# Performance work log

Hardware: AMD Instinct MI355X
Metric: run time of the kernel (lower is better)

## Reference

```python
import jax, jax.numpy as jnp
import numpy as np

N, E, DIN, HID, G, L = 50000, 200000, 128, 128, 64, 6
H1, H2 = 8, 4
EPS_LN, EPS_BN = 1e-5, 1e-5


def setup_inputs() -> dict:
    key = jax.random.key(0)
    ks = iter(jax.random.split(key, 32))
    def nrm(shape, scale=0.05):
        return jax.random.normal(next(ks), shape, dtype=jnp.float32) * scale
    z = lambda *s: jnp.zeros(s, jnp.float32)
    o = lambda *s: jnp.ones(s, jnp.float32)
    return {
        'x': jax.random.normal(next(ks), (N, DIN), dtype=jnp.float32),
        'edge_index': jax.random.randint(next(ks), (2, E), 0, N),
        'batch': jnp.sort(jax.random.randint(next(ks), (N,), 0, G)),
        'W1': nrm((DIN, H1 * HID)), 'a_src1': nrm((H1, HID)), 'a_dst1': nrm((H1, HID)), 'b1': z(H1 * HID),
        'W2': nrm((H1 * HID, H2 * HID)), 'a_src2': nrm((H2, HID)), 'a_dst2': nrm((H2, HID)), 'b2': z(H2 * HID),
        'W3': nrm((H2 * HID, HID)), 'b3': z(HID),
        'wq': nrm((L, HID, HID)), 'bq': z(L, HID), 'wk': nrm((L, HID, HID)), 'bk': z(L, HID),
        'wv': nrm((L, HID, HID)), 'bv': z(L, HID), 'wo': nrm((L, HID, HID)), 'bo': z(L, HID),
        'ln1g': o(L, HID), 'ln1b': z(L, HID), 'ln2g': o(L, HID), 'ln2b': z(L, HID),
        'wf1': nrm((L, HID, 4 * HID)), 'bf1': z(L, 4 * HID), 'wf2': nrm((L, 4 * HID, HID)), 'bf2': z(L, HID),
        'bn1_g': o(2 * HID), 'bn1_b': z(2 * HID),
        'fc1_w': nrm((2 * HID, HID // 2)), 'fc1_b': z(HID // 2),
        'bn2_g': o(HID // 2), 'bn2_b': z(HID // 2),
        'fc2_w': nrm((HID // 2, 2)), 'fc2_b': z(2),
    }


def _ln(x, g, b):
    mu = x.mean(-1, keepdims=True)
    v = ((x - mu) ** 2).mean(-1, keepdims=True)
    return (x - mu) * jax.lax.rsqrt(v + EPS_LN) * g + b


def _gat(x, src, dst, W, a_s, a_d, b, heads):
    # PyG GATConv: message src -> dst, segment softmax over incoming edges per dst.
    h = (x @ W).reshape(x.shape[0], heads, -1)           # [N, H, C]
    e = jax.nn.leaky_relu((h * a_s).sum(-1)[src] + (h * a_d).sum(-1)[dst], 0.2)  # [E, H]
    m = jax.ops.segment_max(e, dst, num_segments=N)
    ex = jnp.exp(e - jnp.where(jnp.isfinite(m), m, 0.0)[dst])
    s = jax.ops.segment_sum(ex, dst, num_segments=N)
    alpha = ex / (s[dst] + 1e-16)
    out = jax.ops.segment_sum(alpha[:, :, None] * h[src], dst, num_segments=N)
    return out.reshape(N, -1) + b


def _forward(x, edge_index, batch, W1, a_src1, a_dst1, b1, W2, a_src2, a_dst2, b2, W3, b3,
             wq, bq, wk, bk, wv, bv, wo, bo, ln1g, ln1b, ln2g, ln2b, wf1, bf1, wf2, bf2,
             bn1_g, bn1_b, fc1_w, fc1_b, bn2_g, bn2_b, fc2_w, fc2_b):
    loop = jnp.arange(N, dtype=edge_index.dtype)
    src = jnp.concatenate([edge_index[0], loop])          # add self-loops (PyG default)
    dst = jnp.concatenate([edge_index[1], loop])
    h = jax.nn.elu(_gat(x, src, dst, W1, a_src1, a_dst1, b1, H1))
    h = jax.nn.elu(_gat(h, src, dst, W2, a_src2, a_dst2, b2, H2))
    # GCNConv with symmetric normalization (self-loops already included)
    deg = jax.ops.segment_sum(jnp.ones(src.shape, h.dtype), dst, num_segments=N)
    dinv = jnp.where(deg > 0, jax.lax.rsqrt(jnp.maximum(deg, 1e-12)), 0.0)
    norm = dinv[src] * dinv[dst]
    h = jax.nn.elu(jax.ops.segment_sum(norm[:, None] * (h @ W3)[src], dst, num_segments=N) + b3)
    # TransformerEncoder over seq_len=1 (h3.unsqueeze(1)): softmax over one key == 1,
    # so MHA output == Wo @ (Wv h + bv) + bo exactly; q/k have no effect on the output.
    for l in range(L):
        sa = (h @ wv[l] + bv[l]) @ wo[l] + bo[l]
        h = _ln(h + sa, ln1g[l], ln1b[l])
        ff = jax.nn.gelu(h @ wf1[l] + bf1[l], approximate=False) @ wf2[l] + bf2[l]
        h = _ln(h + ff, ln2g[l], ln2b[l])
    # global mean / max pool over graphs
    cnt = jax.ops.segment_sum(jnp.ones((N,), h.dtype), batch, num_segments=G)
    hm = jax.ops.segment_sum(h, batch, num_segments=G) / jnp.maximum(cnt, 1.0)[:, None]
    hx = jax.ops.segment_max(h, batch, num_segments=G)
    hx = jnp.where(jnp.isfinite(hx), hx, 0.0)
    hc = jnp.concatenate([hm, hx], axis=1)                # [G, 2*HID]
    bn_s = 1.0 / np.sqrt(1.0 + EPS_BN)                    # eval BN: running stats (0, 1)
    hc = hc * bn_s * bn1_g + bn1_b
    hc = jax.nn.elu(hc @ fc1_w + fc1_b)
    hc = hc * bn_s * bn2_g + bn2_b
    return hc @ fc2_w + fc2_b                             # [G, 2]


def reference(x, edge_index, batch, W1, a_src1, a_dst1, b1, W2, a_src2, a_dst2, b2, W3, b3,
              wq, bq, wk, bk, wv, bv, wo, bo, ln1g, ln1b, ln2g, ln2b, wf1, bf1, wf2, bf2,
              bn1_g, bn1_b, fc1_w, fc1_b, bn2_g, bn2_b, fc2_w, fc2_b):
    return _forward(x, edge_index, batch, W1, a_src1, a_dst1, b1, W2, a_src2, a_dst2, b2, W3, b3,
                    wq, bq, wk, bk, wv, bv, wo, bo, ln1g, ln1b, ln2g, ln2b, wf1, bf1, wf2, bf2,
                    bn1_g, bn1_b, fc1_w, fc1_b, bn2_g, bn2_b, fc2_w, fc2_b)
```

## Files before the change

### kernel.cpp

```cpp
#include <hip/hip_runtime.h>
#include <hip/hip_bf16.h>
#include <math.h>

#define NN 50000
#define EE 200000
#define ET 250000
#define GG 64
#define LL 6

using short8 = __attribute__((ext_vector_type(8))) short;
using f32x4  = __attribute__((ext_vector_type(4))) float;
typedef unsigned short ushortT;

__device__ __forceinline__ float elu1(float x) { return x > 0.f ? x : expm1f(x); }
__device__ __forceinline__ float gelu_exact(float x) {
    return 0.5f * x * (1.f + erff(x * 0.70710678118654752440f));
}
__device__ __forceinline__ short f2bf(float f) {
    __hip_bfloat16 h = __float2bfloat16(f);
    return *reinterpret_cast<short*>(&h);
}
__device__ __forceinline__ float bf2f(ushortT u) {
    return __uint_as_float(((unsigned)u) << 16);
}
__device__ __forceinline__ void accum8(float* acc, float a, uint4 d) {
    acc[0] += a * bf2f((ushortT)(d.x & 0xffff));
    acc[1] += a * bf2f((ushortT)(d.x >> 16));
    acc[2] += a * bf2f((ushortT)(d.y & 0xffff));
    acc[3] += a * bf2f((ushortT)(d.y >> 16));
    acc[4] += a * bf2f((ushortT)(d.z & 0xffff));
    acc[5] += a * bf2f((ushortT)(d.z >> 16));
    acc[6] += a * bf2f((ushortT)(d.w & 0xffff));
    acc[7] += a * bf2f((ushortT)(d.w >> 16));
}

__global__ void count_deg_kernel(const int* __restrict__ ei, int* __restrict__ deg) {
    int e = blockIdx.x * 256 + threadIdx.x;
    if (e >= ET) return;
    int dst = (e < EE) ? ei[EE + e] : (e - EE);
    atomicAdd(&deg[dst], 1);
}

__global__ void scan_kernel(const int* __restrict__ deg, int* __restrict__ row_ptr, int n) {
    __shared__ int s[1024];
    int tid = threadIdx.x;
    const int per = (n + 1023) / 1024;
    int lo = tid * per, hi = min(lo + per, n);
    int sum = 0;
    for (int i = lo; i < hi; i++) sum += deg[i];
    s[tid] = sum;
    __syncthreads();
    for (int off = 1; off < 1024; off <<= 1) {
        int t = (tid >= off) ? s[tid - off] : 0;
        __syncthreads();
        s[tid] += t;
        __syncthreads();
    }
    int run = s[tid] - sum;
    for (int i = lo; i < hi; i++) { row_ptr[i] = run; run += deg[i]; }
    if (tid == 1023) row_ptr[n] = s[1023];
}

__global__ void fill_csr_kernel(const int* __restrict__ ei, const int* __restrict__ row_ptr,
                                int* __restrict__ cursor, int* __restrict__ edge_src) {
    int e = blockIdx.x * 256 + threadIdx.x;
    if (e >= ET) return;
    int src, dst;
    if (e < EE) { src = ei[e]; dst = ei[EE + e]; }
    else        { src = e - EE; dst = e - EE; }
    int pos = atomicAdd(&cursor[dst], 1);
    edge_src[row_ptr[dst] + pos] = src;
}

__global__ void dinv_kernel(const int* __restrict__ row_ptr, float* __restrict__ dinv) {
    int n = blockIdx.x * 256 + threadIdx.x;
    if (n >= NN) return;
    int d = row_ptr[n + 1] - row_ptr[n];
    dinv[n] = (d > 0) ? rsqrtf((float)d) : 0.f;
}

__global__ __launch_bounds__(256) void local_sort_kernel(
    const int* __restrict__ row_ptr, int* __restrict__ perm, int n_nodes) {
    int g = blockIdx.x * 4 + (threadIdx.x >> 6);
    int l = threadIdx.x & 63;
    int node = g * 64 + l;
    if (g * 64 >= n_nodes) return;
    int d = (node < n_nodes) ? (row_ptr[node + 1] - row_ptr[node]) : 0x7fffffff;
    int rank = 0;
#pragma unroll 16
    for (int j = 0; j < 64; j++) {
        int dj = __shfl(d, j);
        rank += (dj < d) || (dj == d && j < l);
    }
    if (node < n_nodes) perm[g * 64 + rank] = node;
}

__global__ void wvwo_kernel(const float* __restrict__ wv, const float* __restrict__ wo,
                            const float* __restrict__ bv, const float* __restrict__ bo,
                            float* __restrict__ Wvo, float* __restrict__ bvo) {
    int l = blockIdx.y;
    const float* Wv = wv + l * 16384;
    const float* Wo = wo + l * 16384;
    int tid = blockIdx.x * 256 + threadIdx.x;
    if (tid < 16384) {
        int r = tid >> 7, c = tid & 127;
        float s = 0.f;
        for (int k = 0; k < 128; k++) s += Wv[r * 128 + k] * Wo[k * 128 + c];
        Wvo[l * 16384 + tid] = s;
    }
    if (blockIdx.x == 0 && threadIdx.x < 128) {
        int c = threadIdx.x;
        float s = bo[l * 128 + c];
        for (int k = 0; k < 128; k++) s += bv[l * 128 + k] * Wo[k * 128 + c];
        bvo[l * 128 + c] = s;
    }
}

__global__ void bprep_kernel(const float* __restrict__ B, short* __restrict__ Bp,
                             int K, int N, int ldb, long srcStride) {
    int layer = blockIdx.y;
    const float* Bsrc = B + srcStride * layer;
    short* Bd = Bp + (size_t)K * N * layer;
    int total = (K >> 5) * (N >> 4) * 64;
    int tid = blockIdx.x * 256 + threadIdx.x;
    if (tid >= total) return;
    int l = tid & 63;
    int rest = tid >> 6;
    int kbc = K >> 5;
    int kb = rest % kbc;
    int c16 = rest / kbc;
    int n = c16 * 16 + (l & 15);
    int kbase = kb * 32 + (l >> 4) * 8;
    short v[8];
#pragma unroll
    for (int j = 0; j < 8; j++) v[j] = f2bf(Bsrc[(size_t)(kbase + j) * ldb + n]);
    *(uint4*)(Bd + (size_t)tid * 8) = *(uint4*)v;
}

__global__ void cast_bf16_kernel(const float* __restrict__ in, short* __restrict__ out, int n4) {
    int i = blockIdx.x * 256 + threadIdx.x;
    if (i >= n4) return;
    float4 v = *(const float4*)(in + (size_t)i * 4);
    short s[4] = { f2bf(v.x), f2bf(v.y), f2bf(v.z), f2bf(v.w) };
    *(uint2*)(out + (size_t)i * 4) = *(uint2*)s;
}

template <int EPI, bool BIAS, bool OUTBF16, int NSPLIT, int KBC,
          bool TMAJ = false, bool ATILE32 = false>
__global__ __launch_bounds__(256) void gemm_bf16_kernel(
    const short* __restrict__ A, const short* __restrict__ Bp,
    const float* __restrict__ bias, void* __restrict__ Cv,
    const float* __restrict__ a_s, const float* __restrict__ a_d,
    float* __restrict__ as_out, float* __restrict__ ad_out, int asH,
    int M, int K, int Nc) {
    __shared__ short Bs[(KBC > 0) ? KBC * 4096 : 8192];
    int t = threadIdx.x;
    int w = t >> 6, l = t & 63;
    int ln = l & 15, lq = l >> 4;
    int MBceil = (M + 63) >> 6;
    int bx = blockIdx.x;
    int xcd = bx & 7, idx = bx >> 3;
    int t2 = idx % NSPLIT;
    int mb = (idx / NSPLIT) * 8 + xcd;
    if (mb >= MBceil) return;
    int bm = mb * 64 + w * 16;
    int arow = bm + ln;
    bool aok = arow < M;
    int rowb = bm + lq * 4;
    const short* Ap = A + (size_t)arow * K + lq * 8;

    auto aload = [&](int kb) -> short8 {
        if (!aok) return (short8){0, 0, 0, 0, 0, 0, 0, 0};
        const short* p;
        if constexpr (ATILE32)
            p = A + ((size_t)kb * M + arow) * 32 + lq * 8;
        else
            p = Ap + kb * 32;
        return *(const short8*)p;
    };

    f32x4 acc[8];
#pragma unroll
    for (int j = 0; j < 8; j++) acc[j] = (f32x4){0.f, 0.f, 0.f, 0.f};

    if constexpr (KBC > 0) {
        {
            const uint4* src = (const uint4*)(Bp + (size_t)t2 * KBC * 4096);
            uint4* dst = (uint4*)Bs;
#pragma unroll
            for (int i = 0; i < KBC * 2; i++)
                dst[i * 256 + t] = src[i * 256 + t];
        }
        short8 af[KBC];
#pragma unroll
        for (int kb = 0; kb < KBC; kb++)
            af[kb] = aload(kb);
        __syncthreads();
#pragma unroll
        for (int kb = 0; kb < KBC; kb++)
#pragma unroll
            for (int ct = 0; ct < 8; ct++) {
                short8 bfr = *(const short8*)(Bs + ((ct * KBC + kb) * 64 + l) * 8);
                acc[ct] = __builtin_amdgcn_mfma_f32_16x16x32_bf16(af[kb], bfr, acc[ct], 0, 0, 0);
            }
    } else {
        int kbc = K >> 5;
        int sct = t >> 5, spart = t & 31;
        auto stage = [&](int buf, int kb) {
            const uint4* src = (const uint4*)(Bp + ((size_t)(t2 * 8 + sct) * kbc + kb) * 512);
            uint4* dst = (uint4*)(Bs + buf * 4096 + sct * 512);
            dst[spart * 2]     = src[spart * 2];
            dst[spart * 2 + 1] = src[spart * 2 + 1];
        };
        stage(0, 0);
        __syncthreads();
        for (int kb = 0; kb < kbc; kb++) {
            if (kb + 1 < kbc) stage((kb + 1) & 1, kb + 1);
            short8 af = aload(kb);
            const short* bsb = Bs + (kb & 1) * 4096;
#pragma unroll
            for (int ct = 0; ct < 8; ct++) {
                short8 bfr = *(const short8*)(bsb + (ct * 64 + l) * 8);
                acc[ct] = __builtin_amdgcn_mfma_f32_16x16x32_bf16(af, bfr, acc[ct], 0, 0, 0);
            }
            __syncthreads();
        }
    }

    if (EPI == 2) {
        const float* asv = a_s + t2 * 128;
        const float* adv = a_d + t2 * 128;
#pragma unroll
        for (int reg = 0; reg < 4; reg++) {
            float vs = 0.f, vd = 0.f;
#pragma unroll
            for (int ct = 0; ct < 8; ct++) {
                int colL = ct * 16 + ln;
                float av = acc[ct][reg];
                vs += av * asv[colL];
                vd += av * adv[colL];
            }
            vs += __shfl_xor(vs, 1); vs += __shfl_xor(vs, 2);
            vs += __shfl_xor(vs, 4); vs += __shfl_xor(vs, 8);
            vd += __shfl_xor(vd, 1); vd += __shfl_xor(vd, 2);
            vd += __shfl_xor(vd, 4); vd += __shfl_xor(vd, 8);
            int row = rowb + reg;
            if (ln == 0 && row < M) {
                as_out[(size_t)row * asH + t2] = vs;
                ad_out[(size_t)row * asH + t2] = vd;
            }
        }
    }
#pragma unroll
    for (int ct = 0; ct < 8; ct++) {
        int col = t2 * 128 + ct * 16 + ln;
        float bv_ = BIAS ? bias[col] : 0.f;
#pragma unroll
        for (int reg = 0; reg < 4; reg++) {
            int row = rowb + reg;
            if (row < M) {
                float v = acc[ct][reg] + bv_;
                if (OUTBF16) {
                    size_t addr;
                    if constexpr (TMAJ)
                        addr = ((size_t)(col >> 5) * M + row) * 32 + (col & 31);
                    else
                        addr = (size_t)row * Nc + col;
                    ((__hip_bfloat16*)Cv)[addr] = __float2bfloat16(v);
                } else {
                    ((float*)Cv)[(size_t)row * Nc + col] = v;
                }
            }
        }
    }
}

#define TS 136
__global__ __launch_bounds__(256) void transformer_fused_kernel(
    const short* __restrict__ Qb, const short* __restrict__ Wvop,
    const float* __restrict__ bvo, const short* __restrict__ wf1p,
    const short* __restrict__ wf2p, const float* __restrict__ bf1,
    const float* __restrict__ bf2, const float* __restrict__ ln1g,
    const float* __restrict__ ln1b, const float* __restrict__ ln2g,
    const float* __restrict__ ln2b, float* __restrict__ fQ, int M) {
    __shared__ short Ts[4][16 * TS];
    int t = threadIdx.x;
    int w = t >> 6, l = t & 63;
    int ln = l & 15, lq = l >> 4;
    int MBceil = (M + 63) >> 6;
    int bx = blockIdx.x;
    int xcd = bx & 7, mb = (bx >> 3) * 8 + xcd;
    if (mb >= MBceil) return;
    int bm = mb * 64 + w * 16;
    int rowb = bm + lq * 4;
    short* Tw = &Ts[w][0];

    ushortT hc[8][4];
#pragma unroll
    for (int ct = 0; ct < 8; ct++) {
        int col = ct * 16 + ln;
#pragma unroll
        for (int reg = 0; reg < 4; reg++) {
            int row = rowb + reg;
            hc[ct][reg] = (row < M) ? ((const ushortT*)Qb)[(size_t)row * 128 + col] : 0;
        }
    }

    auto bounceA = [&](short8* a) {
#pragma unroll
        for (int ct = 0; ct < 8; ct++)
#pragma unroll
            for (int reg = 0; reg < 4; reg++)
                Tw[(lq * 4 + reg) * TS + ct * 16 + ln] = (short)hc[ct][reg];
#pragma unroll
        for (int kb = 0; kb < 4; kb++)
            a[kb] = *(const short8*)(Tw + ln * TS + kb * 32 + lq * 8);
    };
    auto bload = [&](const short* wp, int frag) -> short8 {
        return *(const short8*)(wp + ((size_t)frag * 64 + l) * 8);
    };
    auto lnEpi = [&](f32x4* acc, const float* bias, const float* g,
                     const float* b, bool writeF) {
        float v[8][4];
#pragma unroll
        for (int ct = 0; ct < 8; ct++) {
            float bv_ = bias[ct * 16 + ln];
#pragma unroll
            for (int reg = 0; reg < 4; reg++)
                v[ct][reg] = acc[ct][reg] + bv_ + bf2f(hc[ct][reg]);
        }
#pragma unroll
        for (int reg = 0; reg < 4; reg++) {
            float s = 0.f;
#pragma unroll
            for (int ct = 0; ct < 8; ct++) s += v[ct][reg];
            s += __shfl_xor(s, 1); s += __shfl_xor(s, 2);
            s += __shfl_xor(s, 4); s += __shfl_xor(s, 8);
            float mean = s * (1.f / 128.f);
            float s2 = 0.f;
#pragma unroll
            for (int ct = 0; ct < 8; ct++) { float d = v[ct][reg] - mean; s2 += d * d; }
            s2 += __shfl_xor(s2, 1); s2 += __shfl_xor(s2, 2);
            s2 += __shfl_xor(s2, 4); s2 += __shfl_xor(s2, 8);
            float rstd = rsqrtf(s2 * (1.f / 128.f) + 1e-5f);
            int row = rowb + reg;
#pragma unroll
            for (int ct = 0; ct < 8; ct++) {
                int col = ct * 16 + ln;
                float o = (v[ct][reg] - mean) * rstd * g[col] + b[col];
                hc[ct][reg] = (ushortT)f2bf(o);
                if (writeF && row < M) fQ[(size_t)row * 128 + col] = o;
            }
        }
    };

    for (int lay = 0; lay < LL; lay++) {
        short8 a1[4];
        bounceA(a1);
        const short* wvl = Wvop + (size_t)lay * 16384;
        f32x4 acc1[8];
#pragma unroll
        for (int j = 0; j < 8; j++) acc1[j] = (f32x4){0.f, 0.f, 0.f, 0.f};
#pragma unroll
        for (int kb = 0; kb < 4; kb++)
#pragma unroll
            for (int ct = 0; ct < 8; ct++) {
                short8 bfr = bload(wvl, ct * 4 + kb);
                acc1[ct] = __builtin_amdgcn_mfma_f32_16x16x32_bf16(a1[kb], bfr, acc1[ct], 0, 0, 0);
            }
        lnEpi(acc1, bvo + lay * 128, ln1g + lay * 128, ln1b + lay * 128, false);

        short8 af1[4];
        bounceA(af1);
        const short* w1l = wf1p + (size_t)lay * 65536;
        const short* w2l = wf2p + (size_t)lay * 65536;
        f32x4 acc2[8];
#pragma unroll
        for (int j = 0; j < 8; j++) acc2[j] = (f32x4){0.f, 0.f, 0.f, 0.f};
        for (int kc = 0; kc < 4; kc++) {
            f32x4 acct[8];
#pragma unroll
            for (int j = 0; j < 8; j++) acct[j] = (f32x4){0.f, 0.f, 0.f, 0.f};
#pragma unroll
            for (int kb = 0; kb < 4; kb++)
#pragma unroll
                for (int ct = 0; ct < 8; ct++) {
                    short8 bfr = bload(w1l, kc * 32 + ct * 4 + kb);
                    acct[ct] = __builtin_amdgcn_mfma_f32_16x16x32_bf16(af1[kb], bfr, acct[ct], 0, 0, 0);
                }
            const float* bfc = bf1 + lay * 512 + kc * 128;
#pragma unroll
            for (int ct = 0; ct < 8; ct++) {
                float bv = bfc[ct * 16 + ln];
#pragma unroll
                for (int reg = 0; reg < 4; reg++)
                    Tw[(lq * 4 + reg) * TS + ct * 16 + ln] = f2bf(gelu_exact(acct[ct][reg] + bv));
            }
            short8 a2[4];
#pragma unroll
            for (int kb2 = 0; kb2 < 4; kb2++)
                a2[kb2] = *(const short8*)(Tw + ln * TS + kb2 * 32 + lq * 8);
#pragma unroll
            for (int kb2 = 0; kb2 < 4; kb2++)
#pragma unroll
                for (int ct = 0; ct < 8; ct++) {
                    short8 bfr = bload(w2l, ct * 16 + kc * 4 + kb2);
                    acc2[ct] = __builtin_amdgcn_mfma_f32_16x16x32_bf16(a2[kb2], bfr, acc2[ct], 0, 0, 0);
                }
        }
        lnEpi(acc2, bf2 + lay * 128, ln2g + lay * 128, ln2b + lay * 128, lay == LL - 1);
    }
}

template <int H>
__global__ __launch_bounds__(256) void gat_alpha_kernel(
    const float* __restrict__ as_, const float* __restrict__ ad_,
    const int* __restrict__ row_ptr, const int* __restrict__ edge_src,
    float* __restrict__ exA, float* __restrict__ exS, int n_nodes) {
    const int GS = 64 / H;
    int node = blockIdx.x * 4 + (threadIdx.x >> 6);
    if (node >= n_nodes) return;
    int l = threadIdx.x & 63;
    int h = l / GS;
    int lig = l % GS;
    int start = row_ptr[node];
    int deg = row_ptr[node + 1] - start;
    float adn = ad_[(size_t)node * H + h];
    float m = -1e30f;
    for (int j = lig; j < deg; j += GS) {
        int s = edge_src[start + j];
        float e = as_[(size_t)s * H + h] + adn;
        e = e > 0.f ? e : 0.2f * e;
        m = fmaxf(m, e);
    }
#pragma unroll
    for (int mask = 1; mask < GS; mask <<= 1)
        m = fmaxf(m, __shfl_xor(m, mask));
    float S = 0.f;
    for (int j = lig; j < deg; j += GS) {
        int s = edge_src[start + j];
        float e = as_[(size_t)s * H + h] + adn;
        e = e > 0.f ? e : 0.2f * e;
        float ex = expf(e - m);
        exA[(size_t)h * ET + (start + j)] = ex;
        S += ex;
    }
#pragma unroll
    for (int mask = 1; mask < GS; mask <<= 1)
        S += __shfl_xor(S, mask);
    if (lig == 0) exS[(size_t)h * n_nodes + node] = S;
}

__global__ __launch_bounds__(256) void gat_agg_tiled_kernel(
    const ushortT* __restrict__ hT, const float* __restrict__ exA,
    const float* __restrict__ exS, const float* __restrict__ bias,
    const int* __restrict__ row_ptr, const int* __restrict__ edge_src,
    const int* __restrict__ perm,
    __hip_bfloat16* __restrict__ outT, int n_nodes, int NB) {
    int bx = blockIdx.x;
    int xcd = bx & 7, rest = bx >> 3;
    int tl = rest / NB, nb = rest - tl * NB;
    int tile = tl * 8 + xcd;
    int nl = threadIdx.x >> 2, q = threadIdx.x & 3;
    int idx = nb * 64 + nl;
    if (idx >= n_nodes) return;
    int node = perm[idx];
    int hb = tile >> 2;
    const ushortT* __restrict__ base = hT + (size_t)tile * n_nodes * 32 + q * 8;
    const float* __restrict__ exAh = exA + (size_t)hb * ET;
    int start = row_ptr[node];
    int deg = row_ptr[node + 1] - start;
    float acc[8];
#pragma unroll
    for (int c = 0; c < 8; c++) acc[c] = 0.f;
    for (int j = 0; j < deg; j++) {
        int s = edge_src[start + j];
        float a = exAh[start + j];
        uint4 d = *(const uint4*)(base + (size_t)s * 32);
        accum8(acc, a, d);
    }
    float inv = 1.f / (exS[(size_t)hb * n_nodes + node] + 1e-16f);
    const float* bp = bias + tile * 32 + q * 8;
    short o[8];
#pragma unroll
    for (int c = 0; c < 8; c++)
        o[c] = f2bf(elu1(acc[c] * inv + bp[c]));
    *(uint4*)(outT + ((size_t)tile * n_nodes + node) * 32 + q * 8) = *(uint4*)o;
}

__global__ __launch_bounds__(256, 2) void gcn_agg_kernel(
    const ushortT* __restrict__ hp, const float* __restrict__ dinv,
    const float* __restrict__ b3, const int* __restrict__ row_ptr,
    const int* __restrict__ edge_src,
    __hip_bfloat16* __restrict__ outb, int n_nodes) {
    int node = blockIdx.x * 2 + (threadIdx.x >> 7);
    int c = threadIdx.x & 127;
    if (node >= n_nodes) return;
    int start = row_ptr[node];
    int deg = row_ptr[node + 1] - start;
    float dn = dinv[node];
    float acc = 0.f;
    auto LS = [&](int j) { return edge_src[start + min(j, deg - 1)]; };
    int s0 = LS(0), s1 = LS(1), s2 = LS(2), s3 = LS(3);
    int s4 = LS(4), s5 = LS(5), s6 = LS(6), s7 = LS(7);
    auto HW = [&](int s, int j, float& h, float& w) {
        h = bf2f(hp[(size_t)s * 128 + c]);
        w = (j < deg) ? dinv[s] * dn : 0.f;
    };
    float h0, h1, h2, h3, h4, h5, h6, h7;
    float w0, w1, w2, w3, w4, w5, w6, w7;
    HW(s0, 0, h0, w0); HW(s1, 1, h1, w1); HW(s2, 2, h2, w2); HW(s3, 3, h3, w3);
    HW(s4, 4, h4, w4); HW(s5, 5, h5, w5); HW(s6, 6, h6, w6); HW(s7, 7, h7, w7);
    int j0 = 0;
    while (true) {
        int jn = j0 + 8;
        bool more = jn < deg;
        float g0, g1, g2, g3, g4, g5, g6, g7;
        float v0 = 0.f, v1 = 0.f, v2 = 0.f, v3 = 0.f;
        float v4 = 0.f, v5 = 0.f, v6 = 0.f, v7 = 0.f;
        if (more) {
            int t0 = LS(jn),     t1 = LS(jn + 1), t2 = LS(jn + 2), t3 = LS(jn + 3);
            int t4 = LS(jn + 4), t5 = LS(jn + 5), t6 = LS(jn + 6), t7 = LS(jn + 7);
            HW(t0, jn,     g0, v0); HW(t1, jn + 1, g1, v1);
            HW(t2, jn + 2, g2, v2); HW(t3, jn + 3, g3, v3);
            HW(t4, jn + 4, g4, v4); HW(t5, jn + 5, g5, v5);
            HW(t6, jn + 6, g6, v6); HW(t7, jn + 7, g7, v7);
        }
        acc += w0 * h0 + w1 * h1 + w2 * h2 + w3 * h3
             + w4 * h4 + w5 * h5 + w6 * h6 + w7 * h7;
        if (!more) break;
        h0 = g0; h1 = g1; h2 = g2; h3 = g3;
        h4 = g4; h5 = g5; h6 = g6; h7 = g7;
        w0 = v0; w1 = v1; w2 = v2; w3 = v3;
        w4 = v4; w5 = v5; w6 = v6; w7 = v7;
        j0 = jn;
    }
    outb[(size_t)node * 128 + c] = __float2bfloat16(elu1(acc + b3[c]));
}

__global__ void pool1_kernel(const float* __restrict__ Q, const int* __restrict__ batch,
                             float* __restrict__ psum, float* __restrict__ pmax, int n_nodes) {
    int g = blockIdx.x, seg = blockIdx.y;
    int c = threadIdx.x;
    int lo, hi;
    {
        int l = 0, h = n_nodes;
        while (l < h) { int mid = (l + h) >> 1; if (batch[mid] < g) l = mid + 1; else h = mid; }
        lo = l;
        l = lo; h = n_nodes;
        while (l < h) { int mid = (l + h) >> 1; if (batch[mid] < g + 1) l = mid + 1; else h = mid; }
        hi = l;
    }
    int len = hi - lo;
    int a = lo + (int)((long)len * seg / 8);
    int b = lo + (int)((long)len * (seg + 1) / 8);
    float s = 0.f, mx = -INFINITY;
    for (int n = a; n < b; n++) {
        float v = Q[(size_t)n * 128 + c];
        s += v;
        mx = fmaxf(mx, v);
    }
    psum[(g * 8 + seg) * 128 + c] = s;
    pmax[(g * 8 + seg) * 128 + c] = mx;
}

__global__ void pool2_kernel(const float* __restrict__ psum, const float* __restrict__ pmax,
                             const int* __restrict__ batch,
                             const float* __restrict__ bn1g, const float* __restrict__ bn1b,
                             float* __restrict__ hc, int n_nodes) {
    int g = blockIdx.x;
    int c = threadIdx.x;
    int lo, hi;
    {
        int l = 0, h = n_nodes;
        while (l < h) { int mid = (l + h) >> 1; if (batch[mid] < g) l = mid + 1; else h = mid; }
        lo = l;
        l = lo; h = n_nodes;
        while (l < h) { int mid = (l + h) >> 1; if (batch[mid] < g + 1) l = mid + 1; else h = mid; }
        hi = l;
    }
    int cnt = hi - lo;
    float s = 0.f, mx = -INFINITY;
    for (int seg = 0; seg < 8; seg++) {
        s += psum[(g * 8 + seg) * 128 + c];
        mx = fmaxf(mx, pmax[(g * 8 + seg) * 128 + c]);
    }
    float hm = s / fmaxf((float)cnt, 1.f);
    float hx = (cnt > 0 && isfinite(mx)) ? mx : 0.f;
    const float bn_s = 0.99999500003749968f;
    hc[g * 256 + c]       = hm * bn_s * bn1g[c] + bn1b[c];
    hc[g * 256 + 128 + c] = hx * bn_s * bn1g[128 + c] + bn1b[128 + c];
}

__global__ void head_kernel(const float* __restrict__ hc,
                            const float* __restrict__ fc1w, const float* __restrict__ fc1b,
                            const float* __restrict__ bn2g, const float* __restrict__ bn2b,
                            const float* __restrict__ fc2w, const float* __restrict__ fc2b,
                            float* __restrict__ out) {
    int g = blockIdx.x;
    int j = threadIdx.x;
    const float bn_s = 0.99999500003749968f;
    float acc = fc1b[j];
    for (int i = 0; i < 256; i++) acc += hc[g * 256 + i] * fc1w[i * 64 + j];
    acc = elu1(acc);
    acc = acc * bn_s * bn2g[j] + bn2b[j];
    __shared__ float sv[64];
    sv[j] = acc;
    __syncthreads();
    if (j < 2) {
        float o = fc2b[j];
        for (int i = 0; i < 64; i++) o += sv[i] * fc2w[i * 2 + j];
        out[g * 2 + j] = o;
    }
}

extern "C" void kernel_launch(void* const* d_in, const int* in_sizes, int n_in,
                              void* d_out, int out_size, void* d_ws, size_t ws_size,
                              hipStream_t stream) {
    const float* x    = (const float*)d_in[0];
    const int*   ei   = (const int*)d_in[1];
    const int*   batch= (const int*)d_in[2];
    const float* W1   = (const float*)d_in[3];
    const float* as1  = (const float*)d_in[4];
    const float* ad1  = (const float*)d_in[5];
    const float* b1   = (const float*)d_in[6];
    const float* W2   = (const float*)d_in[7];
    const float* as2  = (const float*)d_in[8];
    const float* ad2  = (const float*)d_in[9];
    const float* b2   = (const float*)d_in[10];
    const float* W3   = (const float*)d_in[11];
    const float* b3   = (const float*)d_in[12];
    const float* wv   = (const float*)d_in[17];
    const float* bv   = (const float*)d_in[18];
    const float* wo   = (const float*)d_in[19];
    const float* bo   = (const float*)d_in[20];
    const float* ln1g = (const float*)d_in[21];
    const float* ln1b = (const float*)d_in[22];
    const float* ln2g = (const float*)d_in[23];
    const float* ln2b = (const float*)d_in[24];
    const float* wf1  = (const float*)d_in[25];
    const float* bf1  = (const float*)d_in[26];
    const float* wf2  = (const float*)d_in[27];
    const float* bf2  = (const float*)d_in[28];
    const float* bn1g = (const float*)d_in[29];
    const float* bn1b = (const float*)d_in[30];
    const float* fc1w = (const float*)d_in[31];
    const float* fc1b = (const float*)d_in[32];
    const float* bn2g = (const float*)d_in[33];
    const float* bn2b = (const float*)d_in[34];
    const float* fc2w = (const float*)d_in[35];
    const float* fc2b = (const float*)d_in[36];
    float* out = (float*)d_out;

    char* wsb = (char*)d_ws;
    short* xb    = (short*)wsb;
    float* exAf  = (float*)wsb;
    float* exSf  = (float*)(wsb + 8000000);
    short* h1t   = (short*)(wsb + 12800000);
    short* h2t   = (short*)(wsb + 12800000);
    short* h3pre = (short*)(wsb + 12800000);
    short* bh1   = (short*)(wsb + 115200000);
    short* bh2   = (short*)(wsb + 115200000);
    float* fQ    = (float*)(wsb + 128000000);
    short* Qb    = (short*)(wsb + 153600000);
    char* tail = wsb + 217600000;
    short* W1p  = (short*)tail;  tail += 262144;
    short* W2p  = (short*)tail;  tail += 1048576;
    short* W3p  = (short*)tail;  tail += 131072;
    short* Wvop = (short*)tail;  tail += 196608;
    short* wf1p = (short*)tail;  tail += 786432;
    short* wf2p = (short*)tail;  tail += 786432;
    float* Wvo  = (float*)tail;  tail += 393216;
    float* bvo  = (float*)tail;  tail += 3072;
    float* fAS  = (float*)tail;  tail += 1600000;
    float* fAD  = (float*)tail;  tail += 1600000;
    float* fDv  = (float*)tail;  tail += 200000;
    float* psum = (float*)tail;  tail += 262144;
    float* pmax = (float*)tail;  tail += 262144;
    float* fHC  = (float*)tail;  tail += 65536;
    int* iDeg   = (int*)tail;    tail += 200000;
    int* iRP    = (int*)tail;    tail += 200004;
    int* iCur   = (int*)tail;    tail += 200000;
    int* iES    = (int*)tail;    tail += 1000000;

    hipMemsetAsync(iDeg, 0, NN * sizeof(int), stream);
    hipMemsetAsync(iCur, 0, NN * sizeof(int), stream);

    count_deg_kernel<<<(ET + 255) / 256, 256, 0, stream>>>(ei, iDeg);
    scan_kernel<<<1, 1024, 0, stream>>>(iDeg, iRP, NN);
    fill_csr_kernel<<<(ET + 255) / 256, 256, 0, stream>>>(ei, iRP, iCur, iES);
    dinv_kernel<<<(NN + 255) / 256, 256, 0, stream>>>(iRP, fDv);
    int* perm = iCur;
    local_sort_kernel<<<(NN / 64 + 4) / 4, 256, 0, stream>>>(iRP, perm, NN);

    wvwo_kernel<<<dim3(64, 6), 256, 0, stream>>>(wv, wo, bv, bo, Wvo, bvo);
    auto bprep = [&](const float* B, short* Bp, int K, int N, int ldb, long sStride, int layers) {
        int total = (K >> 5) * (N >> 4) * 64;
        dim3 grid((total + 255) / 256, layers);
        bprep_kernel<<<grid, 256, 0, stream>>>(B, Bp, K, N, ldb, sStride);
    };
    bprep(W1, W1p, 128, 1024, 1024, 0, 1);
    bprep(W2, W2p, 1024, 512, 512, 0, 1);
    bprep(W3, W3p, 512, 128, 128, 0, 1);
    bprep(Wvo, Wvop, 128, 128, 128, 16384, 6);
    bprep(wf1, wf1p, 128, 512, 512, 65536, 6);
    bprep(wf2, wf2p, 512, 128, 128, 65536, 6);
    cast_bf16_kernel<<<(NN * 128 / 4 + 255) / 256, 256, 0, stream>>>(x, xb, NN * 128 / 4);

    const int MB64 = (NN + 63) / 64;
    const int MBp = ((MB64 + 7) / 8) * 8;
    const int NB = (NN + 63) / 64;

    gemm_bf16_kernel<2, false, true, 8, 4, true, false><<<MBp * 8, 256, 0, stream>>>(
        xb, W1p, nullptr, h1t, as1, ad1, fAS, fAD, 8, NN, 128, 1024);
    gat_alpha_kernel<8><<<(NN + 3) / 4, 256, 0, stream>>>(
        fAS, fAD, iRP, iES, exAf, exSf, NN);
    gat_agg_tiled_kernel<<<4 * NB * 8, 256, 0, stream>>>(
        (const ushortT*)h1t, exAf, exSf, b1, iRP, iES, perm, (__hip_bfloat16*)bh1, NN, NB);
    gemm_bf16_kernel<2, false, true, 4, 0, true, true><<<MBp * 4, 256, 0, stream>>>(
        bh1, W2p, nullptr, h2t, as2, ad2, fAS, fAD, 4, NN, 1024, 512);
    gat_alpha_kernel<4><<<(NN + 3) / 4, 256, 0, stream>>>(
        fAS, fAD, iRP, iES, exAf, exSf, NN);
    gat_agg_tiled_kernel<<<2 * NB * 8, 256, 0, stream>>>(
        (const ushortT*)h2t, exAf, exSf, b2, iRP, iES, perm, (__hip_bfloat16*)bh2, NN, NB);
    gemm_bf16_kernel<0, false, true, 1, 0, false, true><<<MBp, 256, 0, stream>>>(
        bh2, W3p, nullptr, h3pre, nullptr, nullptr, nullptr, nullptr, 0, NN, 512, 128);
    gcn_agg_kernel<<<(NN + 1) / 2, 256, 0, stream>>>(
        (const ushortT*)h3pre, fDv, b3, iRP, iES, (__hip_bfloat16*)Qb, NN);
    transformer_fused_kernel<<<MBp, 256, 0, stream>>>(
        Qb, Wvop, bvo, wf1p, wf2p, bf1, bf2, ln1g, ln1b, ln2g, ln2b, fQ, NN);
    pool1_kernel<<<dim3(GG, 8), 128, 0, stream>>>(fQ, batch, psum, pmax, NN);
    pool2_kernel<<<GG, 128, 0, stream>>>(psum, pmax, batch, bn1g, bn1b, fHC, NN);
    head_kernel<<<GG, 64, 0, stream>>>(fHC, fc1w, fc1b, bn2g, bn2b, fc2w, fc2b, out);
}
```

Before: 1.373 ms.

## Stage transformer weights through double-buffered LDS with async global-to-LDS prefetch

```diff
diff --git a/kernel.cpp b/kernel.cpp
--- a/kernel.cpp
+++ b/kernel.cpp
@@ -32,6 +32,16 @@
     acc[5] += a * bf2f((ushortT)(d.z >> 16));
     acc[6] += a * bf2f((ushortT)(d.w & 0xffff));
     acc[7] += a * bf2f((ushortT)(d.w >> 16));
+}
+
+__device__ __forceinline__ void gl16(const short* g, short* l) {
+#if defined(__has_builtin) && __has_builtin(__builtin_amdgcn_global_load_lds)
+    __builtin_amdgcn_global_load_lds(
+        (const __attribute__((address_space(1))) unsigned int*)g,
+        (__attribute__((address_space(3))) unsigned int*)l, 16, 0, 0);
+#else
+    *(uint4*)l = *(const uint4*)g;
+#endif
 }
 
 __global__ void count_deg_kernel(const int* __restrict__ ei, int* __restrict__ deg) {
@@ -283,6 +293,7 @@
     const float* __restrict__ bf2, const float* __restrict__ ln1g,
     const float* __restrict__ ln1b, const float* __restrict__ ln2g,
     const float* __restrict__ ln2b, float* __restrict__ fQ, int M) {
+    __shared__ short BsD[16384];
     __shared__ short Ts[4][16 * TS];
     int t = threadIdx.x;
     int w = t >> 6, l = t & 63;
@@ -306,6 +317,32 @@
         }
     }
 
+    auto pfLinear = [&](const short* base, int buf) {
+#pragma unroll
+        for (int i = 0; i < 4; i++) {
+            int off = i * 2048 + w * 512;
+            gl16(base + off + l * 8, BsD + buf * 8192 + off);
+        }
+    };
+    auto pfW2 = [&](const short* w2l, int kc, int h, int buf) {
+#pragma unroll
+        for (int i = 0; i < 4; i++) {
+            int frag = ((i + h * 4) << 4) + kc * 4 + w;
+            int slot = i * 4 + w;
+            gl16(w2l + frag * 512 + l * 8, BsD + buf * 8192 + slot * 512);
+        }
+    };
+    auto mfmaHalf = [&](f32x4* acc, int half, short8* a, int buf) {
+        const short* bsb = BsD + buf * 8192;
+#pragma unroll
+        for (int kb = 0; kb < 4; kb++)
+#pragma unroll
+            for (int ct2 = 0; ct2 < 4; ct2++) {
+                short8 bfr = *(const short8*)(bsb + ((ct2 * 4 + kb) * 64 + l) * 8);
+                acc[half * 4 + ct2] =
+                    __builtin_amdgcn_mfma_f32_16x16x32_bf16(a[kb], bfr, acc[half * 4 + ct2], 0, 0, 0);
+            }
+    };
     auto bounceA = [&](short8* a) {
 #pragma unroll
         for (int ct = 0; ct < 8; ct++)
@@ -315,9 +352,6 @@
 #pragma unroll
         for (int kb = 0; kb < 4; kb++)
             a[kb] = *(const short8*)(Tw + ln * TS + kb * 32 + lq * 8);
-    };
-    auto bload = [&](const short* wp, int frag) -> short8 {
-        return *(const short8*)(wp + ((size_t)frag * 64 + l) * 8);
     };
     auto lnEpi = [&](f32x4* acc, const float* bias, const float* g,
                      const float* b, bool writeF) {
@@ -354,26 +388,29 @@
         }
     };
 
+    int cur = 0;
+    pfLinear(Wvop, 0);
+    __syncthreads();
+
     for (int lay = 0; lay < LL; lay++) {
+        const short* wvl = Wvop + (size_t)lay * 16384;
+        const short* w1l = wf1p + (size_t)lay * 65536;
+        const short* w2l = wf2p + (size_t)lay * 65536;
         short8 a1[4];
         bounceA(a1);
-        const short* wvl = Wvop + (size_t)lay * 16384;
         f32x4 acc1[8];
 #pragma unroll
         for (int j = 0; j < 8; j++) acc1[j] = (f32x4){0.f, 0.f, 0.f, 0.f};
-#pragma unroll
-        for (int kb = 0; kb < 4; kb++)
-#pragma unroll
-            for (int ct = 0; ct < 8; ct++) {
-                short8 bfr = bload(wvl, ct * 4 + kb);
-                acc1[ct] = __builtin_amdgcn_mfma_f32_16x16x32_bf16(a1[kb], bfr, acc1[ct], 0, 0, 0);
-            }
+        pfLinear(wvl + 8192, cur ^ 1);
+        mfmaHalf(acc1, 0, a1, cur);
+        __syncthreads(); cur ^= 1;
+        pfLinear(w1l, cur ^ 1);
+        mfmaHalf(acc1, 1, a1, cur);
         lnEpi(acc1, bvo + lay * 128, ln1g + lay * 128, ln1b + lay * 128, false);
-
         short8 af1[4];
         bounceA(af1);
-        const short* w1l = wf1p + (size_t)lay * 65536;
-        const short* w2l = wf2p + (size_t)lay * 65536;
+        __syncthreads(); cur ^= 1;
+
         f32x4 acc2[8];
 #pragma unroll
         for (int j = 0; j < 8; j++) acc2[j] = (f32x4){0.f, 0.f, 0.f, 0.f};
@@ -381,13 +418,11 @@
             f32x4 acct[8];
 #pragma unroll
             for (int j = 0; j < 8; j++) acct[j] = (f32x4){0.f, 0.f, 0.f, 0.f};
-#pragma unroll
-            for (int kb = 0; kb < 4; kb++)
-#pragma unroll
-                for (int ct = 0; ct < 8; ct++) {
-                    short8 bfr = bload(w1l, kc * 32 + ct * 4 + kb);
-                    acct[ct] = __builtin_amdgcn_mfma_f32_16x16x32_bf16(af1[kb], bfr, acct[ct], 0, 0, 0);
-                }
+            pfLinear(w1l + kc * 16384 + 8192, cur ^ 1);
+            mfmaHalf(acct, 0, af1, cur);
+            __syncthreads(); cur ^= 1;
+            pfW2(w2l, kc, 0, cur ^ 1);
+            mfmaHalf(acct, 1, af1, cur);
             const float* bfc = bf1 + lay * 512 + kc * 128;
 #pragma unroll
             for (int ct = 0; ct < 8; ct++) {
@@ -400,13 +435,14 @@
 #pragma unroll
             for (int kb2 = 0; kb2 < 4; kb2++)
                 a2[kb2] = *(const short8*)(Tw + ln * TS + kb2 * 32 + lq * 8);
-#pragma unroll
-            for (int kb2 = 0; kb2 < 4; kb2++)
-#pragma unroll
-                for (int ct = 0; ct < 8; ct++) {
-                    short8 bfr = bload(w2l, ct * 16 + kc * 4 + kb2);
-                    acc2[ct] = __builtin_amdgcn_mfma_f32_16x16x32_bf16(a2[kb2], bfr, acc2[ct], 0, 0, 0);
-                }
+            __syncthreads(); cur ^= 1;
+            pfW2(w2l, kc, 1, cur ^ 1);
+            mfmaHalf(acc2, 0, a2, cur);
+            __syncthreads(); cur ^= 1;
+            if (kc < 3)            pfLinear(w1l + (kc + 1) * 16384, cur ^ 1);
+            else if (lay < LL - 1) pfLinear(Wvop + (size_t)(lay + 1) * 16384, cur ^ 1);
+            mfmaHalf(acc2, 1, a2, cur);
+            __syncthreads(); cur ^= 1;
         }
         lnEpi(acc2, bf2 + lay * 128, ln2g + lay * 128, ln2b + lay * 128, lay == LL - 1);
     }
```

Result: faster. 1.100 ms (-19.9%).
